# Optimization experiments

Hardware: AMD Instinct MI355X
Metric: run time of the kernel (lower is better)

Reference implementation:

```python
import jax, jax.numpy as jnp
import numpy as np

N_NODES = 50000


def spmm(rows, cols, vals, dense):
    # out[i,:] = sum_{e: rows[e]==i} vals[e] * dense[cols[e], :]
    gathered = dense[cols] * vals[:, None]  # [E, D]
    return jax.ops.segment_sum(gathered, rows, num_segments=N_NODES)


def setup_inputs() -> dict:
    key = jax.random.key(0)
    k1, k2, k3, k4, k5, k6 = jax.random.split(key, 6)
    N, E, F, H, C = N_NODES, 800000, 512, 256, 64
    node_features = jax.random.normal(k1, (N, F), dtype=jnp.float32)
    adj_rows = jax.random.randint(k2, (E,), 0, N, dtype=jnp.int32)
    adj_cols = jax.random.randint(k3, (E,), 0, N, dtype=jnp.int32)
    adj_vals = jax.random.uniform(k4, (E,), dtype=jnp.float32)
    W1 = jax.random.normal(k5, (F, H), dtype=jnp.float32) * (1.0 / np.sqrt(F))
    b1 = jnp.zeros((H,), dtype=jnp.float32)
    W2 = jax.random.normal(k6, (H, C), dtype=jnp.float32) * (1.0 / np.sqrt(H))
    b2 = jnp.zeros((C,), dtype=jnp.float32)
    return {"node_features": node_features, "adj_rows": adj_rows,
            "adj_cols": adj_cols, "adj_vals": adj_vals,
            "W1": W1, "b1": b1, "W2": W2, "b2": b2}


def reference(node_features, adj_rows, adj_cols, adj_vals, W1, b1, W2, b2):
    # Layer 1: dense projection then sparse aggregation, then ReLU.
    support1 = node_features @ W1 + b1           # [N, H]
    x = jax.nn.relu(spmm(adj_rows, adj_cols, adj_vals, support1))
    # Dropout is identity in eval mode (training=False).
    # Layer 2
    support2 = x @ W2 + b2                       # [N, C]
    x = spmm(adj_rows, adj_cols, adj_vals, support2)
    return jax.nn.log_softmax(x, axis=1)
```

## Files before the change

kernel.cpp:

```cpp
#include <hip/hip_runtime.h>

#define N_NODES 50000
#define N_EDGES 800000
#define F_IN    512
#define H_DIM   256
#define C_DIM   64
#define MPAD    50048

#define NB      196
#define NCHUNK  49
#define CHUNK   16384
#define BCAP    6144

typedef __bf16 bf16;
typedef __bf16 bf16x4 __attribute__((ext_vector_type(4)));
typedef __bf16 bf16x8 __attribute__((ext_vector_type(8)));
typedef float  f32x4  __attribute__((ext_vector_type(4)));
typedef unsigned int u32;
typedef unsigned char u8;

__device__ __forceinline__ void gl_lds16(const void* g, void* l) {
    __builtin_amdgcn_global_load_lds(
        (const __attribute__((address_space(1))) u32*)g,
        (__attribute__((address_space(3))) u32*)l, 16, 0, 0);
}

__device__ __forceinline__ float unpack_val(u32 pk) {
    return __builtin_bit_cast(float, pk << 16);
}


__global__ __launch_bounds__(1024) void histA_k(const int* __restrict__ rows,
                                                u32* __restrict__ G) {
    __shared__ u32 h[16 * NB];
    int tid = threadIdx.x, wid = tid >> 6;
    for (int i = tid; i < 16 * NB; i += 1024) h[i] = 0;
    __syncthreads();
    int base = blockIdx.x * CHUNK;
    int end = base + CHUNK; if (end > N_EDGES) end = N_EDGES;
    for (int e = base + tid; e < end; e += 1024)
        atomicAdd(&h[wid * NB + (rows[e] >> 8)], 1);
    __syncthreads();
    if (tid < NB) {
        u32 s = 0;
#pragma unroll
        for (int w = 0; w < 16; w++) s += h[w * NB + tid];
        G[tid * NCHUNK + blockIdx.x] = s;
    }
}

__global__ __launch_bounds__(256) void bucket_scan_k(const u32* __restrict__ G,
                                                     u32* __restrict__ bbase,
                                                     int* __restrict__ starts) {
    __shared__ u32 wtot[4];
    int tid = threadIdx.x, wid = tid >> 6, lane = tid & 63;
    u32 tot = 0;
    if (tid < NB) {
#pragma unroll
        for (int c = 0; c < NCHUNK; c++) tot += G[tid * NCHUNK + c];
    }
    u32 incl = tot;
#pragma unroll
    for (int off = 1; off < 64; off <<= 1) {
        u32 u = __shfl_up(incl, off, 64);
        if (lane >= off) incl += u;
    }
    if (lane == 63) wtot[wid] = incl;
    __syncthreads();
    u32 wpre = 0;
#pragma unroll
    for (int w = 0; w < 4; w++)
        if (w < wid) wpre += wtot[w];
    if (tid < NB) bbase[tid] = wpre + incl - tot;
    if (tid == 0) { bbase[NB] = N_EDGES; starts[N_NODES] = N_EDGES; }
}

__global__ __launch_bounds__(64) void chunk_scan_k(u32* __restrict__ G,
                                                   const u32* __restrict__ bbase) {
    int b = blockIdx.x, lane = threadIdx.x;
    u32 v = (lane < NCHUNK) ? G[b * NCHUNK + lane] : 0;
    u32 incl = v;
#pragma unroll
    for (int off = 1; off < 64; off <<= 1) {
        u32 u = __shfl_up(incl, off, 64);
        if (lane >= off) incl += u;
    }
    if (lane < NCHUNK) G[b * NCHUNK + lane] = bbase[b] + incl - v;
}

__global__ __launch_bounds__(1024) void scatterB_k(const int* __restrict__ rows,
                                                   const int* __restrict__ cols,
                                                   const float* __restrict__ vals,
                                                   const u32* __restrict__ G,
                                                   u32* __restrict__ epack,
                                                   u8* __restrict__ lrow) {
    __shared__ u32 cur[NB];
    int tid = threadIdx.x;
    if (tid < NB) cur[tid] = G[tid * NCHUNK + blockIdx.x];
    __syncthreads();
    int base = blockIdx.x * CHUNK;
    int end = base + CHUNK; if (end > N_EDGES) end = N_EDGES;
    for (int e = base + tid; e < end; e += 1024) {
        int r = rows[e];
        unsigned short vb = __builtin_bit_cast(unsigned short, (bf16)vals[e]);
        u32 pk = ((u32)cols[e] << 16) | (u32)vb;
        u32 p = atomicAdd(&cur[r >> 8], 1);
        epack[p] = pk;
        lrow[p] = (u8)(r & 255);
    }
}

__global__ __launch_bounds__(256) void sortC_k(u32* __restrict__ epack,
                                               const u8* __restrict__ lrow,
                                               const u32* __restrict__ bbase,
                                               int* __restrict__ starts) {
    __shared__ u32 edat[BCAP];
    __shared__ u32 sdat[BCAP];
    __shared__ u8  erow[BCAP];
    __shared__ u32 h[4 * 256];
    __shared__ u32 cur[256];
    __shared__ u32 wtot[4];
    int b = blockIdx.x, tid = threadIdx.x, wid = tid >> 6, lane = tid & 63;
    int s = bbase[b];
    int n = bbase[b + 1] - s;
    if (n > BCAP) n = BCAP;
    for (int i = tid; i < n; i += 256) { edat[i] = epack[s + i]; erow[i] = lrow[s + i]; }
    for (int i = tid; i < 1024; i += 256) h[i] = 0;
    __syncthreads();
    for (int i = tid; i < n; i += 256) atomicAdd(&h[wid * 256 + erow[i]], 1);
    __syncthreads();
    u32 tot = h[tid] + h[256 + tid] + h[512 + tid] + h[768 + tid];
    u32 incl = tot;
#pragma unroll
    for (int off = 1; off < 64; off <<= 1) {
        u32 u = __shfl_up(incl, off, 64);
        if (lane >= off) incl += u;
    }
    if (lane == 63) wtot[wid] = incl;
    __syncthreads();
    u32 wpre = 0;
#pragma unroll
    for (int w = 0; w < 4; w++)
        if (w < wid) wpre += wtot[w];
    u32 excl = wpre + incl - tot;
    cur[tid] = excl;
    int grow = b * 256 + tid;
    if (grow < N_NODES) starts[grow] = s + (int)excl;
    __syncthreads();
    for (int i = tid; i < n; i += 256) {
        u32 p = atomicAdd(&cur[erow[i]], 1);
        sdat[p] = edat[i];
    }
    __syncthreads();
    for (int i = tid; i < n; i += 256) epack[s + i] = sdat[i];
}


__global__ __launch_bounds__(256) void tr_w1_k(const float* __restrict__ W,
                                               bf16* __restrict__ Wt) {
    int i = blockIdx.x * 256 + threadIdx.x;
    int k = i >> 8, n = i & 255;
    Wt[n * F_IN + k] = (bf16)W[i];
}

__global__ __launch_bounds__(256) void tr_w2_k(const float* __restrict__ W,
                                               bf16* __restrict__ Wt) {
    int i = blockIdx.x * 256 + threadIdx.x;
    int k = i >> 6, n = i & 63;
    Wt[n * H_DIM + k] = (bf16)W[i];
}


__global__ __launch_bounds__(512) void gemm1_k(const float* __restrict__ A,
                                               const bf16* __restrict__ Bt,
                                               const float* __restrict__ bias,
                                               bf16* __restrict__ C) {
    constexpr int BM = 128, BN = 256, BK = 64;
    __shared__ bf16 As[BM * BK];
    __shared__ bf16 Bs[BN * BK];

    int tid = threadIdx.x;
    int wid = tid >> 6, lane = tid & 63;
    int wr = wid >> 2, wc = wid & 3;
    int bm = blockIdx.x;

    f32x4 acc[4][4];
#pragma unroll
    for (int m = 0; m < 4; m++)
#pragma unroll
        for (int n = 0; n < 4; n++) acc[m][n] = (f32x4){0.f, 0.f, 0.f, 0.f};

    for (int kt = 0; kt < F_IN; kt += BK) {
#pragma unroll
        for (int j = 0; j < 4; j++) {
            int ch = j * 512 + tid;
            int row = ch >> 3, kc = ch & 7;
            gl_lds16(Bt + (size_t)row * F_IN + kt + kc * 8,
                     &Bs[(j * 512 + wid * 64) * 8]);
        }
#pragma unroll
        for (int j = 0; j < 2; j++) {
            int ch = j * 512 + tid;
            int row = ch >> 3, kc = ch & 7;
            int ar = bm * BM + row;
            if (ar >= N_NODES) ar = N_NODES - 1;
            const f32x4* src = (const f32x4*)(A + (size_t)ar * F_IN + kt + kc * 8);
            f32x4 u = src[0], v = src[1];
            bf16x8 o;
            o[0] = (bf16)u[0]; o[1] = (bf16)u[1]; o[2] = (bf16)u[2]; o[3] = (bf16)u[3];
            o[4] = (bf16)v[0]; o[5] = (bf16)v[1]; o[6] = (bf16)v[2]; o[7] = (bf16)v[3];
            *(bf16x8*)&As[(size_t)ch * 8] = o;
        }
        __syncthreads();

        bf16x8 afr[2][4], bfr[2][4];
#pragma unroll
        for (int kk = 0; kk < 2; kk++) {
#pragma unroll
            for (int m = 0; m < 4; m++)
                afr[kk][m] = *(const bf16x8*)&As[(wr * 64 + m * 16 + (lane & 15)) * BK +
                                                 kk * 32 + (lane >> 4) * 8];
#pragma unroll
            for (int n = 0; n < 4; n++)
                bfr[kk][n] = *(const bf16x8*)&Bs[(wc * 64 + n * 16 + (lane & 15)) * BK +
                                                 kk * 32 + (lane >> 4) * 8];
        }
#pragma unroll
        for (int kk = 0; kk < 2; kk++)
#pragma unroll
            for (int m = 0; m < 4; m++)
#pragma unroll
                for (int n = 0; n < 4; n++)
                    acc[m][n] = __builtin_amdgcn_mfma_f32_16x16x32_bf16(
                        afr[kk][m], bfr[kk][n], acc[m][n], 0, 0, 0);
        __syncthreads();
    }

#pragma unroll
    for (int m = 0; m < 4; m++) {
        int row0 = bm * BM + wr * 64 + m * 16 + (lane >> 4) * 4;
#pragma unroll
        for (int n = 0; n < 4; n++) {
            int col = wc * 64 + n * 16 + (lane & 15);
            float bz = bias[col];
#pragma unroll
            for (int r = 0; r < 4; r++) {
                int row = row0 + r;
                if (row < N_NODES)
                    C[(size_t)row * H_DIM + col] = (bf16)(acc[m][n][r] + bz);
            }
        }
    }
}


__global__ __launch_bounds__(256) void gemm2_k(const bf16* __restrict__ A,
                                               const bf16* __restrict__ Bt,
                                               const float* __restrict__ bias,
                                               bf16* __restrict__ C) {
    constexpr int BM = 128, BN = 64, BK = 64;
    __shared__ bf16 As[BM * BK];
    __shared__ bf16 Bs[BN * BK];

    int tid = threadIdx.x;
    int wid = tid >> 6, lane = tid & 63;
    int wr = wid >> 1, wc = wid & 1;
    int bm = blockIdx.x;

    f32x4 acc[4][2];
#pragma unroll
    for (int m = 0; m < 4; m++)
#pragma unroll
        for (int n = 0; n < 2; n++) acc[m][n] = (f32x4){0.f, 0.f, 0.f, 0.f};

    for (int kt = 0; kt < H_DIM; kt += BK) {
#pragma unroll
        for (int j = 0; j < 4; j++) {
            int ch = j * 256 + tid;
            int row = ch >> 3, kc = ch & 7;
            gl_lds16(A + (size_t)(bm * BM + row) * H_DIM + kt + kc * 8,
                     &As[(j * 256 + wid * 64) * 8]);
        }
#pragma unroll
        for (int j = 0; j < 2; j++) {
            int ch = j * 256 + tid;
            int row = ch >> 3, kc = ch & 7;
            gl_lds16(Bt + (size_t)row * H_DIM + kt + kc * 8,
                     &Bs[(j * 256 + wid * 64) * 8]);
        }
        __syncthreads();

        bf16x8 afr[2][4], bfr[2][2];
#pragma unroll
        for (int kk = 0; kk < 2; kk++) {
#pragma unroll
            for (int m = 0; m < 4; m++)
                afr[kk][m] = *(const bf16x8*)&As[(wr * 64 + m * 16 + (lane & 15)) * BK +
                                                 kk * 32 + (lane >> 4) * 8];
#pragma unroll
            for (int n = 0; n < 2; n++)
                bfr[kk][n] = *(const bf16x8*)&Bs[(wc * 32 + n * 16 + (lane & 15)) * BK +
                                                 kk * 32 + (lane >> 4) * 8];
        }
#pragma unroll
        for (int kk = 0; kk < 2; kk++)
#pragma unroll
            for (int m = 0; m < 4; m++)
#pragma unroll
                for (int n = 0; n < 2; n++)
                    acc[m][n] = __builtin_amdgcn_mfma_f32_16x16x32_bf16(
                        afr[kk][m], bfr[kk][n], acc[m][n], 0, 0, 0);
        __syncthreads();
    }

#pragma unroll
    for (int m = 0; m < 4; m++) {
        int row0 = bm * BM + wr * 64 + m * 16 + (lane >> 4) * 4;
#pragma unroll
        for (int n = 0; n < 2; n++) {
            int col = wc * 32 + n * 16 + (lane & 15);
            float bz = bias[col];
#pragma unroll
            for (int r = 0; r < 4; r++) {
                int row = row0 + r;
                if (row < N_NODES)
                    C[(size_t)row * C_DIM + col] = (bf16)(acc[m][n][r] + bz);
            }
        }
    }
}


__global__ __launch_bounds__(256) void spmm1_k(const int* __restrict__ starts,
                                               const u32* __restrict__ epack,
                                               const bf16* __restrict__ s1,
                                               bf16* __restrict__ x16) {
    int wid = threadIdx.x >> 6, lane = threadIdx.x & 63;
    int row = blockIdx.x * 4 + wid;
    if (row >= N_NODES) return;
    int s = starts[row], e = starts[row + 1];
    f32x4 acc = (f32x4){0.f, 0.f, 0.f, 0.f};
    int p = s;
    for (; p + 4 <= e; p += 4) {
        u32 k0 = epack[p], k1 = epack[p + 1], k2 = epack[p + 2], k3 = epack[p + 3];
        float v0 = unpack_val(k0), v1 = unpack_val(k1),
              v2 = unpack_val(k2), v3 = unpack_val(k3);
        bf16x4 g0 = *(const bf16x4*)(s1 + (size_t)(k0 >> 16) * H_DIM + lane * 4);
        bf16x4 g1 = *(const bf16x4*)(s1 + (size_t)(k1 >> 16) * H_DIM + lane * 4);
        bf16x4 g2 = *(const bf16x4*)(s1 + (size_t)(k2 >> 16) * H_DIM + lane * 4);
        bf16x4 g3 = *(const bf16x4*)(s1 + (size_t)(k3 >> 16) * H_DIM + lane * 4);
#pragma unroll
        for (int j = 0; j < 4; j++)
            acc[j] += v0 * (float)g0[j] + v1 * (float)g1[j] +
                      v2 * (float)g2[j] + v3 * (float)g3[j];
    }
    for (; p < e; ++p) {
        u32 k = epack[p];
        float v = unpack_val(k);
        bf16x4 g = *(const bf16x4*)(s1 + (size_t)(k >> 16) * H_DIM + lane * 4);
#pragma unroll
        for (int j = 0; j < 4; j++) acc[j] += v * (float)g[j];
    }
    bf16x4 o;
#pragma unroll
    for (int j = 0; j < 4; j++) o[j] = (bf16)fmaxf(acc[j], 0.f);
    *(bf16x4*)(x16 + (size_t)row * H_DIM + lane * 4) = o;
}


__global__ __launch_bounds__(256) void spmm2_sm_k(const int* __restrict__ starts,
                                                  const u32* __restrict__ epack,
                                                  const bf16* __restrict__ s2,
                                                  float* __restrict__ out) {
    int wid = threadIdx.x >> 6, lane = threadIdx.x & 63;
    int row = blockIdx.x * 4 + wid;
    if (row >= N_NODES) return;
    int s = starts[row], e = starts[row + 1];
    float acc = 0.f;
    int p = s;
    for (; p + 4 <= e; p += 4) {
        u32 k0 = epack[p], k1 = epack[p + 1], k2 = epack[p + 2], k3 = epack[p + 3];
        float g0 = (float)s2[(size_t)(k0 >> 16) * C_DIM + lane];
        float g1 = (float)s2[(size_t)(k1 >> 16) * C_DIM + lane];
        float g2 = (float)s2[(size_t)(k2 >> 16) * C_DIM + lane];
        float g3 = (float)s2[(size_t)(k3 >> 16) * C_DIM + lane];
        acc += unpack_val(k0) * g0 + unpack_val(k1) * g1 +
               unpack_val(k2) * g2 + unpack_val(k3) * g3;
    }
    for (; p < e; ++p) {
        u32 k = epack[p];
        acc += unpack_val(k) * (float)s2[(size_t)(k >> 16) * C_DIM + lane];
    }
    float mx = acc;
#pragma unroll
    for (int off = 32; off >= 1; off >>= 1) mx = fmaxf(mx, __shfl_xor(mx, off, 64));
    float ex = expf(acc - mx);
    float se = ex;
#pragma unroll
    for (int off = 32; off >= 1; off >>= 1) se += __shfl_xor(se, off, 64);
    out[(size_t)row * C_DIM + lane] = (acc - mx) - logf(se);
}


extern "C" void kernel_launch(void* const* d_in, const int* in_sizes, int n_in,
                              void* d_out, int out_size, void* d_ws, size_t ws_size,
                              hipStream_t stream) {
    const float* nf   = (const float*)d_in[0];
    const int*   rows = (const int*)d_in[1];
    const int*   cols = (const int*)d_in[2];
    const float* vals = (const float*)d_in[3];
    const float* W1   = (const float*)d_in[4];
    const float* b1   = (const float*)d_in[5];
    const float* W2   = (const float*)d_in[6];
    const float* b2   = (const float*)d_in[7];
    float* out = (float*)d_out;

    char* w = (char*)d_ws;
    auto alloc = [&](size_t b) { void* p = (void*)w; w += (b + 255) & ~(size_t)255; return p; };

    bf16* x16  = (bf16*)alloc((size_t)MPAD * H_DIM * 2);
    bf16* sup1 = (bf16*)alloc((size_t)N_NODES * H_DIM * 2);
    bf16* sup2 = sup1;
    bf16* W1t = (bf16*)alloc((size_t)H_DIM * F_IN * 2);
    bf16* W2t = (bf16*)alloc((size_t)C_DIM * H_DIM * 2);
    int* starts = (int*)alloc((size_t)(N_NODES + 1) * 4);
    u32* G      = (u32*)alloc((size_t)NB * NCHUNK * 4);
    u32* bbase  = (u32*)alloc((size_t)(NB + 1) * 4);
    u32* epack  = (u32*)alloc((size_t)N_EDGES * 4);
    u8*  lrow   = (u8*)alloc((size_t)N_EDGES);

    histA_k<<<NCHUNK, 1024, 0, stream>>>(rows, G);
    bucket_scan_k<<<1, 256, 0, stream>>>(G, bbase, starts);
    chunk_scan_k<<<NB, 64, 0, stream>>>(G, bbase);
    scatterB_k<<<NCHUNK, 1024, 0, stream>>>(rows, cols, vals, G, epack, lrow);
    sortC_k<<<NB, 256, 0, stream>>>(epack, lrow, bbase, starts);

    tr_w1_k<<<(F_IN * H_DIM) / 256, 256, 0, stream>>>(W1, W1t);
    tr_w2_k<<<(H_DIM * C_DIM) / 256, 256, 0, stream>>>(W2, W2t);

    gemm1_k<<<MPAD / 128, 512, 0, stream>>>(nf, W1t, b1, sup1);
    spmm1_k<<<(N_NODES + 3) / 4, 256, 0, stream>>>(starts, epack, sup1, x16);

    gemm2_k<<<MPAD / 128, 256, 0, stream>>>(x16, W2t, b2, sup2);
    spmm2_sm_k<<<(N_NODES + 3) / 4, 256, 0, stream>>>(starts, epack, sup2, out);

    (void)in_sizes; (void)n_in; (void)out_size; (void)ws_size;
}
```

Measured before the change: 193.5 us.

## Slice layer-1 SpMM by feature columns and fold scan kernels into consumers

The layer-1 SpMM now splits the 256-wide hidden dimension into 8 slices of 32 columns, with blocks ordered slice-major. Each wavefront processes 4 rows, using 4 lane groups that each gather 2 columns from different edges and reduce with shuffles. The intent is to keep each slice's gather working set in L2 and raise parallelism over edges. Separately, the bucket and chunk scan kernels are removed by recomputing prefix sums redundantly inside the scatter and sort kernels, and the two weight transposes are merged into one launch, cutting the launch count. In exchange, each scatter and sort block re-reads the whole histogram, and the gather now issues narrower 4-byte loads per lane.

```diff
diff --git a/kernel.cpp b/kernel.cpp
--- a/kernel.cpp
+++ b/kernel.cpp
@@ -12,7 +12,14 @@
 #define CHUNK   16384
 #define BCAP    6144
 
+#define SLICES  8
+#define SW      32
+#define RPW     4
+#define RPB     16
+#define SPB     (N_NODES / RPB)
+
 typedef __bf16 bf16;
+typedef __bf16 bf16x2 __attribute__((ext_vector_type(2)));
 typedef __bf16 bf16x4 __attribute__((ext_vector_type(4)));
 typedef __bf16 bf16x8 __attribute__((ext_vector_type(8)));
 typedef float  f32x4  __attribute__((ext_vector_type(4)));
@@ -47,45 +54,6 @@
         for (int w = 0; w < 16; w++) s += h[w * NB + tid];
         G[tid * NCHUNK + blockIdx.x] = s;
     }
-}
-
-__global__ __launch_bounds__(256) void bucket_scan_k(const u32* __restrict__ G,
-                                                     u32* __restrict__ bbase,
-                                                     int* __restrict__ starts) {
-    __shared__ u32 wtot[4];
-    int tid = threadIdx.x, wid = tid >> 6, lane = tid & 63;
-    u32 tot = 0;
-    if (tid < NB) {
-#pragma unroll
-        for (int c = 0; c < NCHUNK; c++) tot += G[tid * NCHUNK + c];
-    }
-    u32 incl = tot;
-#pragma unroll
-    for (int off = 1; off < 64; off <<= 1) {
-        u32 u = __shfl_up(incl, off, 64);
-        if (lane >= off) incl += u;
-    }
-    if (lane == 63) wtot[wid] = incl;
-    __syncthreads();
-    u32 wpre = 0;
-#pragma unroll
-    for (int w = 0; w < 4; w++)
-        if (w < wid) wpre += wtot[w];
-    if (tid < NB) bbase[tid] = wpre + incl - tot;
-    if (tid == 0) { bbase[NB] = N_EDGES; starts[N_NODES] = N_EDGES; }
-}
-
-__global__ __launch_bounds__(64) void chunk_scan_k(u32* __restrict__ G,
-                                                   const u32* __restrict__ bbase) {
-    int b = blockIdx.x, lane = threadIdx.x;
-    u32 v = (lane < NCHUNK) ? G[b * NCHUNK + lane] : 0;
-    u32 incl = v;
-#pragma unroll
-    for (int off = 1; off < 64; off <<= 1) {
-        u32 u = __shfl_up(incl, off, 64);
-        if (lane >= off) incl += u;
-    }
-    if (lane < NCHUNK) G[b * NCHUNK + lane] = bbase[b] + incl - v;
 }
 
 __global__ __launch_bounds__(1024) void scatterB_k(const int* __restrict__ rows,
@@ -95,10 +63,32 @@
                                                    u32* __restrict__ epack,
                                                    u8* __restrict__ lrow) {
     __shared__ u32 cur[NB];
-    int tid = threadIdx.x;
-    if (tid < NB) cur[tid] = G[tid * NCHUNK + blockIdx.x];
-    __syncthreads();
-    int base = blockIdx.x * CHUNK;
+    __shared__ u32 wtot[16];
+    int tid = threadIdx.x, wid = tid >> 6, lane = tid & 63;
+    int c = blockIdx.x;
+    u32 tot = 0, pre = 0;
+    if (tid < NB) {
+        for (int cc = 0; cc < NCHUNK; cc++) {
+            u32 v = G[tid * NCHUNK + cc];
+            tot += v;
+            if (cc < c) pre += v;
+        }
+    }
+    u32 incl = tot;
+#pragma unroll
+    for (int off = 1; off < 64; off <<= 1) {
+        u32 u = __shfl_up(incl, off, 64);
+        if (lane >= off) incl += u;
+    }
+    if (lane == 63) wtot[wid] = incl;
+    __syncthreads();
+    u32 wpre = 0;
+#pragma unroll
+    for (int w = 0; w < 16; w++)
+        if (w < wid) wpre += wtot[w];
+    if (tid < NB) cur[tid] = (wpre + incl - tot) + pre;
+    __syncthreads();
+    int base = c * CHUNK;
     int end = base + CHUNK; if (end > N_EDGES) end = N_EDGES;
     for (int e = base + tid; e < end; e += 1024) {
         int r = rows[e];
@@ -112,18 +102,38 @@
 
 __global__ __launch_bounds__(256) void sortC_k(u32* __restrict__ epack,
                                                const u8* __restrict__ lrow,
-                                               const u32* __restrict__ bbase,
+                                               const u32* __restrict__ G,
                                                int* __restrict__ starts) {
     __shared__ u32 edat[BCAP];
     __shared__ u32 sdat[BCAP];
     __shared__ u8  erow[BCAP];
     __shared__ u32 h[4 * 256];
     __shared__ u32 cur[256];
-    __shared__ u32 wtot[4];
+    __shared__ u32 wt1[4], wt2[4];
+    __shared__ u32 sh_s, sh_n;
     int b = blockIdx.x, tid = threadIdx.x, wid = tid >> 6, lane = tid & 63;
-    int s = bbase[b];
-    int n = bbase[b + 1] - s;
+
+    u32 btot = 0;
+    if (tid < NB)
+        for (int cc = 0; cc < NCHUNK; cc++) btot += G[tid * NCHUNK + cc];
+    u32 bincl = btot;
+#pragma unroll
+    for (int off = 1; off < 64; off <<= 1) {
+        u32 u = __shfl_up(bincl, off, 64);
+        if (lane >= off) bincl += u;
+    }
+    if (lane == 63) wt1[wid] = bincl;
+    __syncthreads();
+    u32 bwpre = 0;
+#pragma unroll
+    for (int w = 0; w < 4; w++)
+        if (w < wid) bwpre += wt1[w];
+    if (tid == b) { sh_s = bwpre + bincl - btot; sh_n = btot; }
+    __syncthreads();
+    int s = (int)sh_s;
+    int n = (int)sh_n;
     if (n > BCAP) n = BCAP;
+
     for (int i = tid; i < n; i += 256) { edat[i] = epack[s + i]; erow[i] = lrow[s + i]; }
     for (int i = tid; i < 1024; i += 256) h[i] = 0;
     __syncthreads();
@@ -136,16 +146,17 @@
         u32 u = __shfl_up(incl, off, 64);
         if (lane >= off) incl += u;
     }
-    if (lane == 63) wtot[wid] = incl;
+    if (lane == 63) wt2[wid] = incl;
     __syncthreads();
     u32 wpre = 0;
 #pragma unroll
     for (int w = 0; w < 4; w++)
-        if (w < wid) wpre += wtot[w];
+        if (w < wid) wpre += wt2[w];
     u32 excl = wpre + incl - tot;
     cur[tid] = excl;
     int grow = b * 256 + tid;
     if (grow < N_NODES) starts[grow] = s + (int)excl;
+    if (b == 0 && tid == 0) starts[N_NODES] = N_EDGES;
     __syncthreads();
     for (int i = tid; i < n; i += 256) {
         u32 p = atomicAdd(&cur[erow[i]], 1);
@@ -156,18 +167,19 @@
 }
 
 
-__global__ __launch_bounds__(256) void tr_w1_k(const float* __restrict__ W,
-                                               bf16* __restrict__ Wt) {
+__global__ __launch_bounds__(256) void tr_w_k(const float* __restrict__ W1,
+                                              const float* __restrict__ W2,
+                                              bf16* __restrict__ W1t,
+                                              bf16* __restrict__ W2t) {
     int i = blockIdx.x * 256 + threadIdx.x;
-    int k = i >> 8, n = i & 255;
-    Wt[n * F_IN + k] = (bf16)W[i];
-}
-
-__global__ __launch_bounds__(256) void tr_w2_k(const float* __restrict__ W,
-                                               bf16* __restrict__ Wt) {
-    int i = blockIdx.x * 256 + threadIdx.x;
-    int k = i >> 6, n = i & 63;
-    Wt[n * H_DIM + k] = (bf16)W[i];
+    if (i < F_IN * H_DIM) {
+        int k = i >> 8, n = i & 255;
+        W1t[n * F_IN + k] = (bf16)W1[i];
+    } else {
+        int j = i - F_IN * H_DIM;
+        int k = j >> 6, n = j & 63;
+        W2t[n * H_DIM + k] = (bf16)W2[j];
+    }
 }
 
 
@@ -331,40 +343,40 @@
 }
 
 
-__global__ __launch_bounds__(256) void spmm1_k(const int* __restrict__ starts,
-                                               const u32* __restrict__ epack,
-                                               const bf16* __restrict__ s1,
-                                               bf16* __restrict__ x16) {
-    int wid = threadIdx.x >> 6, lane = threadIdx.x & 63;
-    int row = blockIdx.x * 4 + wid;
-    if (row >= N_NODES) return;
-    int s = starts[row], e = starts[row + 1];
-    f32x4 acc = (f32x4){0.f, 0.f, 0.f, 0.f};
-    int p = s;
-    for (; p + 4 <= e; p += 4) {
-        u32 k0 = epack[p], k1 = epack[p + 1], k2 = epack[p + 2], k3 = epack[p + 3];
-        float v0 = unpack_val(k0), v1 = unpack_val(k1),
-              v2 = unpack_val(k2), v3 = unpack_val(k3);
-        bf16x4 g0 = *(const bf16x4*)(s1 + (size_t)(k0 >> 16) * H_DIM + lane * 4);
-        bf16x4 g1 = *(const bf16x4*)(s1 + (size_t)(k1 >> 16) * H_DIM + lane * 4);
-        bf16x4 g2 = *(const bf16x4*)(s1 + (size_t)(k2 >> 16) * H_DIM + lane * 4);
-        bf16x4 g3 = *(const bf16x4*)(s1 + (size_t)(k3 >> 16) * H_DIM + lane * 4);
-#pragma unroll
-        for (int j = 0; j < 4; j++)
-            acc[j] += v0 * (float)g0[j] + v1 * (float)g1[j] +
-                      v2 * (float)g2[j] + v3 * (float)g3[j];
-    }
-    for (; p < e; ++p) {
-        u32 k = epack[p];
-        float v = unpack_val(k);
-        bf16x4 g = *(const bf16x4*)(s1 + (size_t)(k >> 16) * H_DIM + lane * 4);
-#pragma unroll
-        for (int j = 0; j < 4; j++) acc[j] += v * (float)g[j];
-    }
-    bf16x4 o;
-#pragma unroll
-    for (int j = 0; j < 4; j++) o[j] = (bf16)fmaxf(acc[j], 0.f);
-    *(bf16x4*)(x16 + (size_t)row * H_DIM + lane * 4) = o;
+__global__ __launch_bounds__(256) void spmm1s_k(const int* __restrict__ starts,
+                                                const u32* __restrict__ epack,
+                                                const bf16* __restrict__ s1,
+                                                bf16* __restrict__ x16) {
+    int tid = threadIdx.x, wid = tid >> 6, lane = tid & 63;
+    int g = lane >> 4, d2 = lane & 15;
+    int bid = blockIdx.x;
+    int sl = bid / SPB, rb = bid - sl * SPB;
+    int dimoff = sl * SW + d2 * 2;
+    const bf16* s1d = s1 + dimoff;
+#pragma unroll
+    for (int rr = 0; rr < RPW; rr++) {
+        int row = rb * RPB + wid * RPW + rr;
+        int s = starts[row], e = starts[row + 1];
+        float a0 = 0.f, a1 = 0.f;
+        for (int p = s; p < e; p += 8) {
+            int p0 = p + g, p1 = p + 4 + g;
+            u32 k0 = (p0 < e) ? epack[p0] : 0u;
+            u32 k1 = (p1 < e) ? epack[p1] : 0u;
+            bf16x2 g0 = *(const bf16x2*)(s1d + (size_t)(k0 >> 16) * H_DIM);
+            bf16x2 g1 = *(const bf16x2*)(s1d + (size_t)(k1 >> 16) * H_DIM);
+            float v0 = unpack_val(k0), v1 = unpack_val(k1);
+            a0 += v0 * (float)g0[0] + v1 * (float)g1[0];
+            a1 += v0 * (float)g0[1] + v1 * (float)g1[1];
+        }
+        a0 += __shfl_xor(a0, 16, 64); a0 += __shfl_xor(a0, 32, 64);
+        a1 += __shfl_xor(a1, 16, 64); a1 += __shfl_xor(a1, 32, 64);
+        if (g == 0) {
+            bf16x2 o;
+            o[0] = (bf16)fmaxf(a0, 0.f);
+            o[1] = (bf16)fmaxf(a1, 0.f);
+            *(bf16x2*)(x16 + (size_t)row * H_DIM + dimoff) = o;
+        }
+    }
 }
 
 
@@ -425,21 +437,17 @@
     bf16* W2t = (bf16*)alloc((size_t)C_DIM * H_DIM * 2);
     int* starts = (int*)alloc((size_t)(N_NODES + 1) * 4);
     u32* G      = (u32*)alloc((size_t)NB * NCHUNK * 4);
-    u32* bbase  = (u32*)alloc((size_t)(NB + 1) * 4);
     u32* epack  = (u32*)alloc((size_t)N_EDGES * 4);
     u8*  lrow   = (u8*)alloc((size_t)N_EDGES);
 
     histA_k<<<NCHUNK, 1024, 0, stream>>>(rows, G);
-    bucket_scan_k<<<1, 256, 0, stream>>>(G, bbase, starts);
-    chunk_scan_k<<<NB, 64, 0, stream>>>(G, bbase);
     scatterB_k<<<NCHUNK, 1024, 0, stream>>>(rows, cols, vals, G, epack, lrow);
-    sortC_k<<<NB, 256, 0, stream>>>(epack, lrow, bbase, starts);
-
-    tr_w1_k<<<(F_IN * H_DIM) / 256, 256, 0, stream>>>(W1, W1t);
-    tr_w2_k<<<(H_DIM * C_DIM) / 256, 256, 0, stream>>>(W2, W2t);
+    sortC_k<<<NB, 256, 0, stream>>>(epack, lrow, G, starts);
+
+    tr_w_k<<<(F_IN * H_DIM + H_DIM * C_DIM) / 256, 256, 0, stream>>>(W1, W2, W1t, W2t);
 
     gemm1_k<<<MPAD / 128, 512, 0, stream>>>(nf, W1t, b1, sup1);
-    spmm1_k<<<(N_NODES + 3) / 4, 256, 0, stream>>>(starts, epack, sup1, x16);
+    spmm1s_k<<<SLICES * SPB, 256, 0, stream>>>(starts, epack, sup1, x16);
 
     gemm2_k<<<MPAD / 128, 256, 0, stream>>>(x16, W2t, b2, sup2);
     spmm2_sm_k<<<(N_NODES + 3) / 4, 256, 0, stream>>>(starts, epack, sup2, out);
```

Result: slower. 255.0 us (+31.8%).
